# Performance work log

Hardware: AMD Instinct MI355X
Metric: run time of the kernel (lower is better)

## Reference

```python
import jax, jax.numpy as jnp
import numpy as np


def setup_inputs() -> dict:
    key = jax.random.key(0)
    ks = jax.random.split(key, 8)
    B, N, H, W, K, C = 32, 256, 14, 14, 8, 1000
    sc = 0.05  # small init scale for numerical sanity
    return {
        "x": jax.random.normal(ks[0], (B, N, H, W), jnp.float32),
        "conv_w": jax.random.normal(ks[1], (K, N), jnp.float32) * sc,          # 1x1 conv N->K, no bias
        "dimred_w": jax.random.normal(ks[2], (K, N, N, H, W), jnp.float32) * sc,  # grouped (H,W) conv: [group, out_m, in_n, H, W]
        "dimred_b": jax.random.normal(ks[3], (K, N), jnp.float32) * sc,
        "Wo_w": jax.random.normal(ks[4], (K, C, N), jnp.float32) * sc,          # grouped 1x1 conv1d
        "Wo_b": jax.random.normal(ks[5], (K, C), jnp.float32) * sc,
        "Wg_w": jax.random.normal(ks[6], (K, N), jnp.float32) * sc,
        "Wg_b": jax.random.normal(ks[7], (K,), jnp.float32) * sc,
    }


def reference(x, conv_w, dimred_w, dimred_b, Wo_w, Wo_b, Wg_w, Wg_b):
    # x: [B,N,H,W]
    # attention maps: 1x1 conv (no bias) + Softmax2d (softmax over channels per pixel)
    ah = jnp.einsum('bnhw,kn->bkhw', x, conv_w)
    ah = jax.nn.softmax(ah, axis=1)  # [B,K,H,W]

    # Orthogonality loss, computed WITHOUT materializing the K^2 repeated tensors.
    # torch: sum_{i,j} ||A_i A_j^T||_F^2 = tr((sum_i A_i^T A_i)^2) = ||G||_F^2,
    # with A_i = ah[:,i] of shape [H,W] and G = sum_i A_i^T A_i (symmetric [W,W]).
    G = jnp.einsum('bkhw,bkhv->bwv', ah, ah)          # [B,W,W]
    loss1 = jnp.sum(G * G, axis=(1, 2))               # [B]
    # torch: sum(ah @ ah^T) = sum_{k,w} (sum_h ah[k,h,w])^2
    s = jnp.sum(ah, axis=2)                           # [B,K,W]
    loss2 = jnp.sum(s * s, axis=(1, 2))               # [B]
    loss = (loss1 - loss2)[:, None]                   # [B,1]

    # Attended features: ah repeated over N * x repeated over K, kept factored as [B,K,N,H,W]
    ah_out = ah[:, :, None, :, :] * x[:, None, :, :, :]   # [B,K,N,H,W]
    # grouped full-spatial conv -> [B,K,N] (torch squeezes to [B,K*N,1])
    dim_red = jnp.einsum('bknhw,kmnhw->bkm', ah_out, dimred_w) + dimred_b  # [B,K,N]

    hyp = jnp.einsum('bkn,kcn->bkc', dim_red, Wo_w) + Wo_b                # [B,K,num_classes]
    conf = jnp.tanh(jnp.einsum('bkn,kn->bk', dim_red, Wg_w) + Wg_b)[..., None]  # [B,K,1]
    return hyp, conf, loss
```

## Files before the change

### kernel.cpp

```cpp
#include <hip/hip_runtime.h>
#include <math.h>

#define B_  32
#define N_  256
#define K_  8
#define HW_ 196
#define C_  1000
#define D_  50176
#define WK_ 12845056

#define WS_AH   0
#define WS_DR   50176
#define WS_PART 115712
#define WS_ABF  6538240

#define NCH 49
#define CHD 1024
#define NPH 4

typedef __attribute__((ext_vector_type(8))) short short8;
typedef __attribute__((ext_vector_type(4))) float f32x4;
typedef unsigned short bf16u;

__device__ __forceinline__ unsigned pk2(float a, float b) {
  unsigned ua = __builtin_bit_cast(unsigned, a);
  unsigned ub = __builtin_bit_cast(unsigned, b);
  ua = (ua + 0x7fffu + ((ua >> 16) & 1u)) >> 16;
  ub = (ub + 0x7fffu + ((ub >> 16) & 1u)) & 0xffff0000u;
  return ub | ua;
}

__global__ __launch_bounds__(256) void k_front(const float* __restrict__ x,
                                               const float* __restrict__ cw,
                                               float* __restrict__ ws,
                                               float* __restrict__ out) {
  const int b = blockIdx.x, t = threadIdx.x;
  __shared__ float cwl[K_][N_];
  __shared__ float AH[K_][HW_ + 4];
  __shared__ float red[256];
#pragma unroll
  for (int i = 0; i < 8; ++i) {
    const int idx = i*256 + t;
    cwl[idx >> 8][idx & 255] = cw[idx];
  }
  __syncthreads();
  if (t < HW_) {
    float acc[K_];
#pragma unroll
    for (int k = 0; k < K_; ++k) acc[k] = 0.f;
    const float* xb = x + (size_t)b*D_ + t;
#pragma unroll 4
    for (int n = 0; n < N_; ++n) {
      const float xv = xb[(size_t)n*HW_];
#pragma unroll
      for (int k = 0; k < K_; ++k) acc[k] = fmaf(xv, cwl[k][n], acc[k]);
    }
    float m = acc[0];
#pragma unroll
    for (int k = 1; k < K_; ++k) m = fmaxf(m, acc[k]);
    float s = 0.f;
#pragma unroll
    for (int k = 0; k < K_; ++k) { acc[k] = __expf(acc[k] - m); s += acc[k]; }
    const float inv = 1.f / s;
#pragma unroll
    for (int k = 0; k < K_; ++k) {
      const float a = acc[k] * inv;
      AH[k][t] = a;
      ws[WS_AH + (b*K_ + k)*HW_ + t] = a;
    }
  }
  __syncthreads();
  float l = 0.f;
  if (t < HW_) {
    const int w = t / 14, v2 = t % 14;
    float g = 0.f;
#pragma unroll
    for (int k = 0; k < K_; ++k)
#pragma unroll
      for (int h = 0; h < 14; ++h)
        g = fmaf(AH[k][h*14 + w], AH[k][h*14 + v2], g);
    l = g * g;
  }
  if (t < 112) {
    const int k2 = t / 14, w = t % 14;
    float s = 0.f;
#pragma unroll
    for (int h = 0; h < 14; ++h) s += AH[k2][h*14 + w];
    l -= s * s;
  }
  red[t] = l;
  __syncthreads();
  for (int s2 = 128; s2 > 0; s2 >>= 1) { if (t < s2) red[t] += red[t + s2]; __syncthreads(); }
  if (t == 0) out[256256 + b] = red[0];
}

__global__ __launch_bounds__(256) void k_amat(const float* __restrict__ x,
                                              const float* __restrict__ ah,
                                              bf16u* __restrict__ abf) {
  const int chunk = blockIdx.x, b = blockIdx.y;
  const int t = threadIdx.x;
  __shared__ float ahl[K_][HW_ + 4];
  if (t < HW_) {
#pragma unroll
    for (int k = 0; k < K_; ++k) ahl[k][t] = ah[(b*K_ + k)*HW_ + t];
  }
  const int d = chunk*CHD + t*4;
  const float4 xv = *(const float4*)(x + (size_t)b*D_ + d);
  int h0 = d % HW_;
  int h1 = h0 + 1; if (h1 >= HW_) h1 -= HW_;
  int h2 = h0 + 2; if (h2 >= HW_) h2 -= HW_;
  int h3 = h0 + 3; if (h3 >= HW_) h3 -= HW_;
  __syncthreads();
#pragma unroll
  for (int k = 0; k < K_; ++k) {
    uint2 v;
    v.x = pk2(xv.x*ahl[k][h0], xv.y*ahl[k][h1]);
    v.y = pk2(xv.z*ahl[k][h2], xv.w*ahl[k][h3]);
    *(uint2*)(abf + (size_t)(b*K_ + k)*D_ + d) = v;
  }
}

__global__ __launch_bounds__(256, 2) void k_dimred(const float* __restrict__ dw,
                                                   const bf16u* __restrict__ abf,
                                                   float* __restrict__ part) {
  const int bid = blockIdx.x;
  const int c    = bid % NCH;
  const int band = bid / NCH;
  const int mg   = band & 3;
  const int k    = band >> 2;
  const int t = threadIdx.x;
  const int lane = t & 63, wv = t >> 6;
  const int r = lane & 15, g = lane >> 4;
  const int h = wv & 1, q = wv >> 1;

  __shared__ __align__(16) char Wb[2][16*2048];

  uint4 ar[16];
  {
    const bf16u* ab = abf + ((size_t)((h*16 + r)*K_ + k))*D_ + c*CHD + q*512 + g*8;
#pragma unroll
    for (int s = 0; s < 16; ++s) ar[s] = *(const uint4*)(ab + s*32);
  }

  const float* wbase = dw + (size_t)k*WK_ + (size_t)(mg*64)*D_ + c*CHD + t*4;
  const int rbase = r*2048;
  const int rswz  = (r & 7) << 4;

  f32x4 wr[16];

  auto load_ph = [&](int p) {
    const float* wp = wbase + (size_t)(p*16)*D_;
#pragma unroll
    for (int i = 0; i < 16; ++i) wr[i] = *(const f32x4*)(wp + (size_t)i*D_);
  };
  auto store_ph = [&](int buf) {
    char* lb = &Wb[buf][0];
#pragma unroll
    for (int i = 0; i < 16; ++i) {
      uint2 v;
      v.x = pk2(wr[i].x, wr[i].y);
      v.y = pk2(wr[i].z, wr[i].w);
      *(uint2*)(lb + i*2048 + ((t*8) ^ ((i & 7) << 4))) = v;
    }
  };

  load_ph(0);
  store_ph(0);
  __syncthreads();

  for (int p = 0; p < NPH; ++p) {
    const int cur = p & 1;
    if (p < NPH - 1) load_ph(p + 1);
    f32x4 acc = {0.f, 0.f, 0.f, 0.f};
    const char* lb = &Wb[cur][0] + rbase;
#pragma unroll
    for (int s = 0; s < 16; ++s) {
      const short8 wf = *(const short8*)(lb + ((q*1024 + s*64 + g*16) ^ rswz));
      const short8 af = __builtin_bit_cast(short8, ar[s]);
      acc = __builtin_amdgcn_mfma_f32_16x16x32_bf16(af, wf, acc, 0, 0, 0);
    }
    {
      const int tm = mg*4 + p;
      float* po = part + ((size_t)(((k*16 + tm)*NCH + c)*2 + q)*2 + h)*256;
#pragma unroll
      for (int rr = 0; rr < 4; ++rr) po[(g*4 + rr)*16 + r] = acc[rr];
    }
    if (p < NPH - 1) store_ph(cur ^ 1);
    __syncthreads();
  }
}

__global__ __launch_bounds__(256) void k_reduce(const float* __restrict__ part,
                                                float* __restrict__ dr) {
  const int tg = blockIdx.x*256 + threadIdx.x;
  const int m = tg & 255, k = (tg >> 8) & 7, b = tg >> 11;
  const int tm = m >> 4, ml = m & 15;
  const int h = b >> 4, bl = b & 15;
  const float* p = part + ((size_t)(k*16 + tm)*(NCH*4) + h)*256 + bl*16 + ml;
  float s = 0.f;
  for (int c = 0; c < NCH; ++c) {
    s += p[(size_t)(c*4 + 0)*256];
    s += p[(size_t)(c*4 + 2)*256];
  }
  dr[tg] = s;
}

__global__ __launch_bounds__(256) void k_out(const float* __restrict__ dr,
                                             const float* __restrict__ db,
                                             const float* __restrict__ Wo,
                                             const float* __restrict__ Wob,
                                             const float* __restrict__ Wg,
                                             const float* __restrict__ Wgb,
                                             float* __restrict__ out) {
  const int ct = blockIdx.x, k = blockIdx.y;
  const int t = threadIdx.x;
  __shared__ float Wl[32][257];
  __shared__ float dl[256][36];
#pragma unroll
  for (int i = 0; i < 32; ++i) {
    const int e = i*256 + t;
    const int row = e >> 8, col = e & 255;
    const int c = ct*32 + row;
    Wl[row][col] = (c < C_) ? Wo[((size_t)(k*C_ + c))*N_ + col] : 0.f;
  }
#pragma unroll
  for (int i = 0; i < 32; ++i) {
    const int e = i*256 + t;
    const int n = e & 255, b = e >> 8;
    dl[n][b] = dr[(b*K_ + k)*N_ + n] + db[k*N_ + n];
  }
  __syncthreads();
  const int tc = t & 31, tg = t >> 5;
  const int c = ct*32 + tc;
  float a0=0.f, a1=0.f, a2=0.f, a3=0.f;
#pragma unroll 8
  for (int n = 0; n < N_; ++n) {
    const float wvv = Wl[tc][n];
    const float4 dv = *(const float4*)&dl[n][tg*4];
    a0 = fmaf(wvv, dv.x, a0);
    a1 = fmaf(wvv, dv.y, a1);
    a2 = fmaf(wvv, dv.z, a2);
    a3 = fmaf(wvv, dv.w, a3);
  }
  if (c < C_) {
    const float bias = Wob[k*C_ + c];
    out[((size_t)(tg*4 + 0)*K_ + k)*C_ + c] = a0 + bias;
    out[((size_t)(tg*4 + 1)*K_ + k)*C_ + c] = a1 + bias;
    out[((size_t)(tg*4 + 2)*K_ + k)*C_ + c] = a2 + bias;
    out[((size_t)(tg*4 + 3)*K_ + k)*C_ + c] = a3 + bias;
  }
  if (ct == 0 && t < B_) {
    float s = Wgb[k];
    for (int n = 0; n < N_; ++n) s = fmaf(dl[n][t], Wg[k*N_ + n], s);
    out[256000 + t*K_ + k] = tanhf(s);
  }
}

extern "C" void kernel_launch(void* const* d_in, const int* in_sizes, int n_in,
                              void* d_out, int out_size, void* d_ws, size_t ws_size,
                              hipStream_t stream) {
  const float* x   = (const float*)d_in[0];
  const float* cw  = (const float*)d_in[1];
  const float* dw  = (const float*)d_in[2];
  const float* db  = (const float*)d_in[3];
  const float* Wo  = (const float*)d_in[4];
  const float* Wob = (const float*)d_in[5];
  const float* Wg  = (const float*)d_in[6];
  const float* Wgb = (const float*)d_in[7];
  float* out = (float*)d_out;
  float* ws  = (float*)d_ws;
  bf16u* abf = (bf16u*)(ws + WS_ABF);

  k_front<<<32, 256, 0, stream>>>(x, cw, ws, out);
  k_amat<<<dim3(NCH, B_), 256, 0, stream>>>(x, ws + WS_AH, abf);
  k_dimred<<<NCH*4*K_, 256, 0, stream>>>(dw, abf, ws + WS_PART);
  k_reduce<<<256, 256, 0, stream>>>(ws + WS_PART, ws + WS_DR);
  k_out<<<dim3(32, 8), 256, 0, stream>>>(ws + WS_DR, db, Wo, Wob, Wg, Wgb, out);
}
```

Baseline: 171.8 us.

## Halve dimred weight staging per phase to raise occupancy, coalesce partial stores and reduce

The weight tile staged per phase in k_dimred is split in half (8 rows of 16 per phase, over 8 phases), which halves the LDS buffer and the register staging array. This allows 3 blocks per CU instead of 2, giving more latency hiding for the weight stream. The MFMA accumulator now spans two phases before it is written. Partial results are stored lane-contiguously, and k_reduce is reorganised so each block sums one (k, m-tile) with coalesced reads and fewer blocks. The cost is more phase iterations and barriers, and more register pressure under the tighter launch bound.

```diff
diff --git a/kernel.cpp b/kernel.cpp
--- a/kernel.cpp
+++ b/kernel.cpp
@@ -16,7 +16,7 @@
 
 #define NCH 49
 #define CHD 1024
-#define NPH 4
+#define NPH 8
 
 typedef __attribute__((ext_vector_type(8))) short short8;
 typedef __attribute__((ext_vector_type(4))) float f32x4;
@@ -120,7 +120,7 @@
   }
 }
 
-__global__ __launch_bounds__(256, 2) void k_dimred(const float* __restrict__ dw,
+__global__ __launch_bounds__(256, 3) void k_dimred(const float* __restrict__ dw,
                                                    const bf16u* __restrict__ abf,
                                                    float* __restrict__ part) {
   const int bid = blockIdx.x;
@@ -133,36 +133,38 @@
   const int r = lane & 15, g = lane >> 4;
   const int h = wv & 1, q = wv >> 1;
 
-  __shared__ __align__(16) char Wb[2][16*2048];
+  __shared__ __align__(16) char Wb[2][16*1024];
 
   uint4 ar[16];
   {
-    const bf16u* ab = abf + ((size_t)((h*16 + r)*K_ + k))*D_ + c*CHD + q*512 + g*8;
-#pragma unroll
-    for (int s = 0; s < 16; ++s) ar[s] = *(const uint4*)(ab + s*32);
-  }
-
-  const float* wbase = dw + (size_t)k*WK_ + (size_t)(mg*64)*D_ + c*CHD + t*4;
-  const int rbase = r*2048;
-  const int rswz  = (r & 7) << 4;
-
-  f32x4 wr[16];
+    const bf16u* ab = abf + ((size_t)((h*16 + r)*K_ + k))*D_ + c*CHD + q*256 + g*8;
+#pragma unroll
+    for (int i = 0; i < 16; ++i) ar[i] = *(const uint4*)(ab + (i >> 3)*512 + (i & 7)*32);
+  }
+
+  const int th = t >> 7, tl = t & 127;
+  const float* wbase = dw + (size_t)k*WK_ + (size_t)(mg*64 + th)*D_ + c*CHD + tl*4;
+  f32x4 wr[8];
 
   auto load_ph = [&](int p) {
-    const float* wp = wbase + (size_t)(p*16)*D_;
-#pragma unroll
-    for (int i = 0; i < 16; ++i) wr[i] = *(const f32x4*)(wp + (size_t)i*D_);
+    const float* wp = wbase + (size_t)((p >> 1)*16)*D_ + (p & 1)*512;
+#pragma unroll
+    for (int s = 0; s < 8; ++s) wr[s] = *(const f32x4*)(wp + (size_t)(2*s)*D_);
   };
   auto store_ph = [&](int buf) {
     char* lb = &Wb[buf][0];
 #pragma unroll
-    for (int i = 0; i < 16; ++i) {
+    for (int s = 0; s < 8; ++s) {
+      const int row = 2*s + th;
       uint2 v;
-      v.x = pk2(wr[i].x, wr[i].y);
-      v.y = pk2(wr[i].z, wr[i].w);
-      *(uint2*)(lb + i*2048 + ((t*8) ^ ((i & 7) << 4))) = v;
+      v.x = pk2(wr[s].x, wr[s].y);
+      v.y = pk2(wr[s].z, wr[s].w);
+      *(uint2*)(lb + row*1024 + ((tl*8) ^ ((row & 7) << 4))) = v;
     }
   };
+
+  f32x4 acc = {0.f, 0.f, 0.f, 0.f};
+  const int swz = (r & 7) << 4;
 
   load_ph(0);
   store_ph(0);
@@ -171,19 +173,19 @@
   for (int p = 0; p < NPH; ++p) {
     const int cur = p & 1;
     if (p < NPH - 1) load_ph(p + 1);
-    f32x4 acc = {0.f, 0.f, 0.f, 0.f};
-    const char* lb = &Wb[cur][0] + rbase;
-#pragma unroll
-    for (int s = 0; s < 16; ++s) {
-      const short8 wf = *(const short8*)(lb + ((q*1024 + s*64 + g*16) ^ rswz));
-      const short8 af = __builtin_bit_cast(short8, ar[s]);
+    const char* lb = &Wb[cur][0] + r*1024;
+#pragma unroll
+    for (int s = 0; s < 8; ++s) {
+      const short8 wf = *(const short8*)(lb + ((q*512 + s*64 + g*16) ^ swz));
+      const short8 af = __builtin_bit_cast(short8, ar[cur*8 + s]);
       acc = __builtin_amdgcn_mfma_f32_16x16x32_bf16(af, wf, acc, 0, 0, 0);
     }
-    {
-      const int tm = mg*4 + p;
+    if (p & 1) {
+      const int tm = mg*4 + (p >> 1);
       float* po = part + ((size_t)(((k*16 + tm)*NCH + c)*2 + q)*2 + h)*256;
 #pragma unroll
-      for (int rr = 0; rr < 4; ++rr) po[(g*4 + rr)*16 + r] = acc[rr];
+      for (int rr = 0; rr < 4; ++rr) po[rr*64 + lane] = acc[rr];
+      acc = (f32x4){0.f, 0.f, 0.f, 0.f};
     }
     if (p < NPH - 1) store_ph(cur ^ 1);
     __syncthreads();
@@ -192,17 +194,20 @@
 
 __global__ __launch_bounds__(256) void k_reduce(const float* __restrict__ part,
                                                 float* __restrict__ dr) {
-  const int tg = blockIdx.x*256 + threadIdx.x;
-  const int m = tg & 255, k = (tg >> 8) & 7, b = tg >> 11;
-  const int tm = m >> 4, ml = m & 15;
-  const int h = b >> 4, bl = b & 15;
-  const float* p = part + ((size_t)(k*16 + tm)*(NCH*4) + h)*256 + bl*16 + ml;
-  float s = 0.f;
+  const int blk = blockIdx.x;
+  const int k = blk >> 4, tm = blk & 15;
+  const int t = threadIdx.x;
+  const float* base = part + (size_t)(k*16 + tm)*NCH*4*256;
+  float a0 = 0.f, a1 = 0.f;
   for (int c = 0; c < NCH; ++c) {
-    s += p[(size_t)(c*4 + 0)*256];
-    s += p[(size_t)(c*4 + 2)*256];
-  }
-  dr[tg] = s;
+    const float* pc = base + c*4*256;
+    a0 += pc[t]       + pc[512 + t];
+    a1 += pc[256 + t] + pc[768 + t];
+  }
+  const int rr = t >> 6, g = (t >> 4) & 3, r = t & 15;
+  const int m = tm*16 + r;
+  dr[((g*4 + rr)*K_ + k)*N_ + m]        = a0;
+  dr[((16 + g*4 + rr)*K_ + k)*N_ + m]   = a1;
 }
 
 __global__ __launch_bounds__(256) void k_out(const float* __restrict__ dr,
@@ -274,6 +279,6 @@
   k_front<<<32, 256, 0, stream>>>(x, cw, ws, out);
   k_amat<<<dim3(NCH, B_), 256, 0, stream>>>(x, ws + WS_AH, abf);
   k_dimred<<<NCH*4*K_, 256, 0, stream>>>(dw, abf, ws + WS_PART);
-  k_reduce<<<256, 256, 0, stream>>>(ws + WS_PART, ws + WS_DR);
+  k_reduce<<<128, 256, 0, stream>>>(ws + WS_PART, ws + WS_DR);
   k_out<<<dim3(32, 8), 256, 0, stream>>>(ws + WS_DR, db, Wo, Wob, Wg, Wgb, out);
 }
```

Measured after the change: 175.9 us. +2.4%, slower.

## Split front kernel into parallel logits and softmax-loss kernels; coalesce partial-sum layout

Applied to the files above, without the earlier changes.

The front kernel computed all K logits per batch in only 32 blocks. It is now split into a logits kernel over (B,K) with 256 blocks and a separate softmax/loss kernel, so the N-long reduction runs across more CUs. The dimred partial-sum stores now go straight to lane-contiguous addresses, and the reduce kernel reads them coalesced and scatters into the dr layout. This adds one kernel launch and a workspace round trip for the logits, and x is reread 8 times (once per k).

```diff
diff --git a/kernel.cpp b/kernel.cpp
--- a/kernel.cpp
+++ b/kernel.cpp
@@ -13,6 +13,7 @@
 #define WS_DR   50176
 #define WS_PART 115712
 #define WS_ABF  6538240
+#define WS_LOG  9749504
 
 #define NCH 49
 #define CHD 1024
@@ -30,41 +31,39 @@
   return ub | ua;
 }
 
-__global__ __launch_bounds__(256) void k_front(const float* __restrict__ x,
-                                               const float* __restrict__ cw,
-                                               float* __restrict__ ws,
-                                               float* __restrict__ out) {
+__global__ __launch_bounds__(256) void k_logits(const float* __restrict__ x,
+                                                const float* __restrict__ cw,
+                                                float* __restrict__ ws) {
+  const int b = blockIdx.x, k = blockIdx.y;
+  const int t = threadIdx.x;
+  __shared__ float cwl[N_];
+  cwl[t] = cw[k*N_ + t];
+  __syncthreads();
+  if (t < HW_) {
+    const float* xb = x + (size_t)b*D_ + t;
+    float acc = 0.f;
+#pragma unroll 8
+    for (int n = 0; n < N_; ++n) acc = fmaf(xb[(size_t)n*HW_], cwl[n], acc);
+    ws[WS_LOG + (b*K_ + k)*HW_ + t] = acc;
+  }
+}
+
+__global__ __launch_bounds__(256) void k_smloss(float* __restrict__ ws,
+                                                float* __restrict__ out) {
   const int b = blockIdx.x, t = threadIdx.x;
-  __shared__ float cwl[K_][N_];
   __shared__ float AH[K_][HW_ + 4];
   __shared__ float red[256];
-#pragma unroll
-  for (int i = 0; i < 8; ++i) {
-    const int idx = i*256 + t;
-    cwl[idx >> 8][idx & 255] = cw[idx];
-  }
-  __syncthreads();
-  if (t < HW_) {
-    float acc[K_];
-#pragma unroll
-    for (int k = 0; k < K_; ++k) acc[k] = 0.f;
-    const float* xb = x + (size_t)b*D_ + t;
-#pragma unroll 4
-    for (int n = 0; n < N_; ++n) {
-      const float xv = xb[(size_t)n*HW_];
-#pragma unroll
-      for (int k = 0; k < K_; ++k) acc[k] = fmaf(xv, cwl[k][n], acc[k]);
-    }
-    float m = acc[0];
-#pragma unroll
-    for (int k = 1; k < K_; ++k) m = fmaxf(m, acc[k]);
+  if (t < HW_) {
+    float v[K_]; float m = -1e30f;
+#pragma unroll
+    for (int k = 0; k < K_; ++k) { v[k] = ws[WS_LOG + (b*K_ + k)*HW_ + t]; m = fmaxf(m, v[k]); }
     float s = 0.f;
 #pragma unroll
-    for (int k = 0; k < K_; ++k) { acc[k] = __expf(acc[k] - m); s += acc[k]; }
+    for (int k = 0; k < K_; ++k) { v[k] = __expf(v[k] - m); s += v[k]; }
     const float inv = 1.f / s;
 #pragma unroll
     for (int k = 0; k < K_; ++k) {
-      const float a = acc[k] * inv;
+      const float a = v[k] * inv;
       AH[k][t] = a;
       ws[WS_AH + (b*K_ + k)*HW_ + t] = a;
     }
@@ -183,7 +182,7 @@
       const int tm = mg*4 + p;
       float* po = part + ((size_t)(((k*16 + tm)*NCH + c)*2 + q)*2 + h)*256;
 #pragma unroll
-      for (int rr = 0; rr < 4; ++rr) po[(g*4 + rr)*16 + r] = acc[rr];
+      for (int rr = 0; rr < 4; ++rr) po[rr*64 + lane] = acc[rr];
     }
     if (p < NPH - 1) store_ph(cur ^ 1);
     __syncthreads();
@@ -192,17 +191,20 @@
 
 __global__ __launch_bounds__(256) void k_reduce(const float* __restrict__ part,
                                                 float* __restrict__ dr) {
-  const int tg = blockIdx.x*256 + threadIdx.x;
-  const int m = tg & 255, k = (tg >> 8) & 7, b = tg >> 11;
-  const int tm = m >> 4, ml = m & 15;
-  const int h = b >> 4, bl = b & 15;
-  const float* p = part + ((size_t)(k*16 + tm)*(NCH*4) + h)*256 + bl*16 + ml;
-  float s = 0.f;
+  const int blk = blockIdx.x;
+  const int k = blk >> 4, tm = blk & 15;
+  const int t = threadIdx.x;
+  const float* base = part + (size_t)(k*16 + tm)*NCH*4*256;
+  float a0 = 0.f, a1 = 0.f;
   for (int c = 0; c < NCH; ++c) {
-    s += p[(size_t)(c*4 + 0)*256];
-    s += p[(size_t)(c*4 + 2)*256];
-  }
-  dr[tg] = s;
+    const float* pc = base + c*4*256;
+    a0 += pc[t]       + pc[512 + t];
+    a1 += pc[256 + t] + pc[768 + t];
+  }
+  const int rr = t >> 6, g = (t >> 4) & 3, r = t & 15;
+  const int m = tm*16 + r;
+  dr[((g*4 + rr)*K_ + k)*N_ + m]        = a0;
+  dr[((16 + g*4 + rr)*K_ + k)*N_ + m]   = a1;
 }
 
 __global__ __launch_bounds__(256) void k_out(const float* __restrict__ dr,
@@ -271,9 +273,10 @@
   float* ws  = (float*)d_ws;
   bf16u* abf = (bf16u*)(ws + WS_ABF);
 
-  k_front<<<32, 256, 0, stream>>>(x, cw, ws, out);
+  k_logits<<<dim3(32, 8), 256, 0, stream>>>(x, cw, ws);
+  k_smloss<<<32, 256, 0, stream>>>(ws, out);
   k_amat<<<dim3(NCH, B_), 256, 0, stream>>>(x, ws + WS_AH, abf);
   k_dimred<<<NCH*4*K_, 256, 0, stream>>>(dw, abf, ws + WS_PART);
-  k_reduce<<<256, 256, 0, stream>>>(ws + WS_PART, ws + WS_DR);
+  k_reduce<<<128, 256, 0, stream>>>(ws + WS_PART, ws + WS_DR);
   k_out<<<dim3(32, 8), 256, 0, stream>>>(ws + WS_DR, db, Wo, Wob, Wg, Wgb, out);
 }
```

Measured after the change: 157.6 us. -8.3%, faster.
